# Kernel optimization log

Hardware: AMD Instinct MI355X
Metric: run time of the kernel (lower is better)

Reference implementation:

```python
import jax, jax.numpy as jnp
import numpy as np

B, H, L = 8, 256, 8192

def setup_inputs() -> dict:
    key = jax.random.key(0)
    k1, k2, k3 = jax.random.split(key, 3)
    u = jax.random.normal(k1, (B, H, L), dtype=jnp.float32)
    K = jax.random.normal(k2, (H, L), dtype=jnp.float32)
    # D ~ uniform_ring with min=max=1.0, field='real' -> random signs on unit ring
    D = jnp.where(jax.random.uniform(k3, (H,)) < 0.5, -1.0, 1.0).astype(jnp.float32)
    return {"u": u, "K": K, "D": D}

def reference(u, K, D):
    # FFT-based circular long convolution per channel: y = ifft(fft(u) * fft(K)).real
    u_s = jnp.fft.fft(u, axis=-1)            # (B,H,L) complex
    k_s = jnp.fft.fft(K, axis=-1)            # (H,L)   complex
    y = jnp.fft.ifft(u_s * k_s[None], axis=-1).real  # (B,H,L)
    y = y + D[None, :, None] * u             # skip connection D*u
    y = jnp.tanh(y)
    return y
```

## Files before the change

### kernel.cpp

```cpp
#include <hip/hip_runtime.h>
#include <math.h>


#define LL 8192
#define NT 512
#define HH 256
#define TWO_PI 6.2831853071795864f
#define CP8  0.92387953251129f
#define SP8  0.38268343236509f
#define CP4  0.70710678118654752f
#define SP4  0.70710678118654752f

__device__ __forceinline__ int SW(int e) {
    return e ^ ((e >> 4) & 0x18) ^ ((e >> 5) & 0x07);
}
__device__ __forceinline__ int SW2(int e) {
    return e ^ (((e >> 5) & 7) << 2);
}
__device__ __forceinline__ float fast_tanh(float x) {
    float e = __expf(2.0f * x);
    return 1.0f - 2.0f / (e + 1.0f);
}

template<int JT>
__device__ __forceinline__ void fill_pyr_cs(float c0, float s0, float Er, float Ei,
                                            float* twr, float* twi) {
    const int off = (1 << JT) - 1;
    twr[off] = c0; twi[off] = s0;
    #pragma unroll
    for (int m = 1; m < (1 << JT); ++m) {
        const float pr = twr[off + m - 1], pi = twi[off + m - 1];
        twr[off + m] = pr * Er - pi * Ei;
        twi[off + m] = pr * Ei + pi * Er;
    }
    #pragma unroll
    for (int j = JT - 1; j >= 0; --j) {
        #pragma unroll
        for (int m = 0; m < (1 << j); ++m) {
            const float a = twr[(2 << j) - 1 + m], b = twi[(2 << j) - 1 + m];
            twr[(1 << j) - 1 + m] = a * a - b * b;
            twi[(1 << j) - 1 + m] = 2.0f * a * b;
        }
    }
}
template<int JT>
__device__ __forceinline__ void fill_pyr(float ang0, float Er, float Ei,
                                         float* twr, float* twi) {
    float s, c;
    __sincosf(ang0, &s, &c);
    fill_pyr_cs<JT>(c, s, Er, Ei, twr, twi);
}

template<int R2>
__device__ __forceinline__ void dif_apply(float* xr, float* xi,
                                          const float* twr, const float* twi) {
    #pragma unroll
    for (int j = R2 - 1; j >= 0; --j) {
        #pragma unroll
        for (int q = 0; q < (1 << (R2 - 1)); ++q) {
            const int mm = q & ((1 << j) - 1);
            const int m0 = ((q >> j) << (j + 1)) | mm;
            const int m1 = m0 + (1 << j);
            const float wr = twr[(1 << j) - 1 + mm], wi = twi[(1 << j) - 1 + mm];
            const float ar = xr[m0], ai = xi[m0], br = xr[m1], bi = xi[m1];
            xr[m0] = ar + br; xi[m0] = ai + bi;
            const float dr = ar - br, di = ai - bi;
            xr[m1] = dr * wr - di * wi;
            xi[m1] = dr * wi + di * wr;
        }
    }
}
template<int R2>
__device__ __forceinline__ void dit_apply(float* xr, float* xi,
                                          const float* twr, const float* twi) {
    #pragma unroll
    for (int j = 0; j < R2; ++j) {
        #pragma unroll
        for (int q = 0; q < (1 << (R2 - 1)); ++q) {
            const int mm = q & ((1 << j) - 1);
            const int m0 = ((q >> j) << (j + 1)) | mm;
            const int m1 = m0 + (1 << j);
            const float wr = twr[(1 << j) - 1 + mm], wi = twi[(1 << j) - 1 + mm];
            const float br = xr[m1] * wr - xi[m1] * wi;
            const float bi = xr[m1] * wi + xi[m1] * wr;
            const float ar = xr[m0], ai = xi[m0];
            xr[m0] = ar + br; xi[m0] = ai + bi;
            xr[m1] = ar - br; xi[m1] = ai - bi;
        }
    }
}


__device__ __forceinline__ void fwd_A(float* xr, float* xi, int tid,
                                      float* re, float* im) {
    float twr[15], twi[15];
    fill_pyr<3>(-(TWO_PI / 8192.0f) * (float)tid, CP8, -SP8, twr, twi);
    dif_apply<4>(xr, xi, twr, twi);
    #pragma unroll
    for (int m = 0; m < 16; ++m) {
        const int p = SW(tid + (m << 9));
        re[p] = xr[m]; im[p] = xi[m];
    }
}

template<bool INV>
__device__ __forceinline__ void mid_M1(float* re, float* im, int lane, int wv) {
    float twr[7], twi[7];
    const float sgn = INV ? 1.0f : -1.0f;
    fill_pyr<2>(sgn * (TWO_PI / 512.0f) * (float)lane, CP4, sgn * SP4, twr, twi);
    #pragma unroll
    for (int r = 0; r < 2; ++r) {
        const int base = (((wv << 1) | r) << 9) + lane;
        float ar[8], ai[8];
        #pragma unroll
        for (int j = 0; j < 8; ++j) {
            const int p = SW(base + (j << 6));
            ar[j] = re[p]; ai[j] = im[p];
        }
        if (INV) dit_apply<3>(ar, ai, twr, twi);
        else     dif_apply<3>(ar, ai, twr, twi);
        #pragma unroll
        for (int j = 0; j < 8; ++j) {
            const int p = SW(base + (j << 6));
            re[p] = ar[j]; im[p] = ai[j];
        }
    }
}

template<bool INV>
__device__ __forceinline__ void mid_M2(float* re, float* im, int lane, int wv) {
    float twr[7], twi[7];
    const float sgn = INV ? 1.0f : -1.0f;
    fill_pyr<2>(sgn * (TWO_PI / 64.0f) * (float)(lane & 7), CP4, sgn * SP4, twr, twi);
    const int sub = ((lane >> 3) << 6) + (lane & 7);
    #pragma unroll
    for (int r = 0; r < 2; ++r) {
        const int base = (((wv << 1) | r) << 9) + sub;
        float ar[8], ai[8];
        #pragma unroll
        for (int j = 0; j < 8; ++j) {
            const int p = SW(base + (j << 3));
            ar[j] = re[p]; ai[j] = im[p];
        }
        if (INV) dit_apply<3>(ar, ai, twr, twi);
        else     dif_apply<3>(ar, ai, twr, twi);
        #pragma unroll
        for (int j = 0; j < 8; ++j) {
            const int p = SW(base + (j << 3));
            re[p] = ar[j]; im[p] = ai[j];
        }
    }
}

__global__ __launch_bounds__(NT, 4) void conv_kernel(const float* __restrict__ u,
                                                     const float2* __restrict__ Kf,
                                                     float* __restrict__ out) {
    __shared__ float re[LL];
    __shared__ float im[LL];
    const int tid = threadIdx.x;
    const int h = blockIdx.x & (HH - 1);
    const int pr_ = blockIdx.x >> 8;
    const size_t off0 = ((size_t)(pr_ * 2) * HH + h) * LL;
    const size_t off1 = off0 + (size_t)HH * LL;
    const float* u0 = u + off0;
    const float* u1 = u + off1;

    float xr[16], xi[16];
    #pragma unroll
    for (int m = 0; m < 16; ++m) {
        xr[m] = u0[tid + (m << 9)];
        xi[m] = u1[tid + (m << 9)];
    }
    fwd_A(xr, xi, tid, re, im);
    __syncthreads();

    const int lane = tid & 63, wv = tid >> 6;
    const int c0 = (wv << 1);

    float kwr[2][8], kwi[2][8];
    #pragma unroll
    for (int r = 0; r < 2; ++r) {
        const int eb = ((c0 | r) << 9) + (lane << 3);
        const float4* kp = (const float4*)(Kf + (size_t)h * LL + eb);
        #pragma unroll
        for (int jj = 0; jj < 4; ++jj) {
            const float4 v = kp[jj];
            kwr[r][2 * jj] = v.x;     kwi[r][2 * jj] = v.y;
            kwr[r][2 * jj + 1] = v.z; kwi[r][2 * jj + 1] = v.w;
        }
    }

    mid_M1<false>(re, im, lane, wv);
    mid_M2<false>(re, im, lane, wv);

    {
        float twd_r[7], twd_i[7], twu_r[7], twu_i[7];
        fill_pyr_cs<2>(1.0f, 0.0f, CP4, -SP4, twd_r, twd_i);
        fill_pyr_cs<2>(1.0f, 0.0f, CP4, SP4, twu_r, twu_i);
        #pragma unroll
        for (int r = 0; r < 2; ++r) {
            const int eb = ((c0 | r) << 9) + (lane << 3);
            float yr[8], yi[8];
            #pragma unroll
            for (int j = 0; j < 8; ++j) {
                const int p = SW(eb + j);
                yr[j] = re[p]; yi[j] = im[p];
            }
            dif_apply<3>(yr, yi, twd_r, twd_i);
            #pragma unroll
            for (int j = 0; j < 8; ++j) {
                const float a = yr[j], b = yi[j];
                yr[j] = a * kwr[r][j] - b * kwi[r][j];
                yi[j] = a * kwi[r][j] + b * kwr[r][j];
            }
            dit_apply<3>(yr, yi, twu_r, twu_i);
            #pragma unroll
            for (int j = 0; j < 8; ++j) {
                const int p = SW(eb + j);
                re[p] = yr[j]; im[p] = yi[j];
            }
        }
    }

    mid_M2<true>(re, im, lane, wv);
    mid_M1<true>(re, im, lane, wv);
    __syncthreads();

    {
        float twr[15], twi[15];
        #pragma unroll
        for (int m = 0; m < 16; ++m) {
            const int p = SW(tid + (m << 9));
            xr[m] = re[p]; xi[m] = im[p];
        }
        fill_pyr<3>((TWO_PI / 8192.0f) * (float)tid, CP8, SP8, twr, twi);
        dit_apply<4>(xr, xi, twr, twi);
    }
    float* o0 = out + off0;
    float* o1 = out + off1;
    #pragma unroll
    for (int m = 0; m < 16; ++m) {
        const int n = tid + (m << 9);
        o0[n] = fast_tanh(xr[m]);
        o1[n] = fast_tanh(xi[m]);
    }
}

__global__ __launch_bounds__(256) void kfftF_kernel(const float* __restrict__ K,
                                                    const float* __restrict__ D,
                                                    float2* __restrict__ Kf) {
    __shared__ float re[2048];
    __shared__ float im[2048];
    const int b = blockIdx.x;
    const int h = b >> 2, cq = b & 3;
    const int tid = threadIdx.x;
    const float* Kr = K + (size_t)h * LL;

    float xr[8], xi[8];
    #pragma unroll
    for (int j = 0; j < 8; ++j) {
        const int m = tid + (j << 8);
        const float A  = Kr[m];
        const float Bv = Kr[m + 2048];
        const float C  = Kr[m + 4096];
        const float E  = Kr[m + 6144];
        if (cq == 0) {
            xr[j] = A + C + Bv + E; xi[j] = 0.0f;
        } else {
            float sn, cs;
            __sincosf(-(TWO_PI / 8192.0f) * (float)m, &sn, &cs);
            if (cq == 1) {
                const float dif = A + C - Bv - E;
                const float c2 = cs * cs - sn * sn, s2 = 2.0f * cs * sn;
                xr[j] = dif * c2; xi[j] = dif * s2;
            } else {
                const float p_ = A - C, q_ = Bv - E;
                if (cq == 2) {
                    xr[j] = p_ * cs + q_ * sn; xi[j] = p_ * sn - q_ * cs;
                } else {
                    const float c2 = cs * cs - sn * sn, s2 = 2.0f * cs * sn;
                    const float c3 = cs * c2 - sn * s2, s3 = cs * s2 + sn * c2;
                    xr[j] = p_ * c3 - q_ * s3; xi[j] = p_ * s3 + q_ * c3;
                }
            }
        }
    }
    {
        float twr[7], twi[7];
        fill_pyr<2>(-(TWO_PI / 2048.0f) * (float)tid, CP4, -SP4, twr, twi);
        dif_apply<3>(xr, xi, twr, twi);
    }
    #pragma unroll
    for (int j = 0; j < 8; ++j) {
        const int p = SW2(tid + (j << 8));
        re[p] = xr[j]; im[p] = xi[j];
    }
    __syncthreads();
    {
        const int t_ = tid & 31, sub = tid >> 5;
        float twr[7], twi[7];
        fill_pyr<2>(-(TWO_PI / 256.0f) * (float)t_, CP4, -SP4, twr, twi);
        const int be = (sub << 8) + t_;
        float ar[8], ai[8];
        #pragma unroll
        for (int j = 0; j < 8; ++j) {
            const int p = SW2(be + (j << 5));
            ar[j] = re[p]; ai[j] = im[p];
        }
        dif_apply<3>(ar, ai, twr, twi);
        #pragma unroll
        for (int j = 0; j < 8; ++j) {
            const int p = SW2(be + (j << 5));
            re[p] = ar[j]; im[p] = ai[j];
        }
    }
    {
        const int blk = tid >> 2, r = tid & 3;
        float twr[7], twi[7];
        fill_pyr<2>(-(TWO_PI / 32.0f) * (float)r, CP4, -SP4, twr, twi);
        const int eb = (blk << 5) + r;
        float yr[8], yi[8];
        #pragma unroll
        for (int j = 0; j < 8; ++j) {
            const int p = SW2(eb + (j << 2));
            yr[j] = re[p]; yi[j] = im[p];
        }
        dif_apply<3>(yr, yi, twr, twi);
        const float s2_ = (r < 2) ? 1.0f : -1.0f;
        #pragma unroll
        for (int j = 0; j < 8; ++j) {
            const float vr = __shfl_xor(yr[j], 2);
            const float vi = __shfl_xor(yi[j], 2);
            const float tr = fmaf(yr[j], s2_, vr);
            const float ti = fmaf(yi[j], s2_, vi);
            yr[j] = (r == 3) ? ti : tr;
            yi[j] = (r == 3) ? -tr : ti;
        }
        const float s1_ = (r & 1) ? -1.0f : 1.0f;
        #pragma unroll
        for (int j = 0; j < 8; ++j) {
            const float vr = __shfl_xor(yr[j], 1);
            const float vi = __shfl_xor(yi[j], 1);
            yr[j] = fmaf(yr[j], s1_, vr);
            yi[j] = fmaf(yi[j], s1_, vi);
        }
        const float dh = D[h];
        const float invN = 1.0f / (float)LL;
        float2* baseo = Kf + (size_t)h * LL + (cq << 11);
        #pragma unroll
        for (int j = 0; j < 8; ++j) {
            baseo[eb + (j << 2)] = make_float2((yr[j] + dh) * invN, yi[j] * invN);
        }
    }
}

extern "C" void kernel_launch(void* const* d_in, const int* in_sizes, int n_in,
                              void* d_out, int out_size, void* d_ws, size_t ws_size,
                              hipStream_t stream) {
    const float* u = (const float*)d_in[0];
    const float* K = (const float*)d_in[1];
    const float* D = (const float*)d_in[2];
    float* out = (float*)d_out;
    float2* Kf = (float2*)d_ws;

    kfftF_kernel<<<dim3(4 * HH), dim3(256), 0, stream>>>(K, D, Kf);
    conv_kernel<<<dim3(4 * HH), dim3(NT), 0, stream>>>(u, Kf, out);
}
```

Measured before the change: 148.8 us.

## Process two batch pairs per block, reusing Kf spectrum and twiddles

Each conv_kernel block now handles two (batch-pair, channel) instances in a loop, halving the grid. The frequency-domain kernel coefficients are loaded once and reused across both instances. The forward mid-stage twiddles are also reused for the inverse pass via a conjugating DIT variant, which cuts twiddle recomputation. Launch bounds drop from 4 to 2 waves/SIMD-occupancy hint, trading parallelism (512 blocks) for fewer redundant loads and per-block setup.

```diff
diff --git a/kernel.cpp b/kernel.cpp
--- a/kernel.cpp
+++ b/kernel.cpp
@@ -89,6 +89,25 @@
         }
     }
 }
+template<int R2>
+__device__ __forceinline__ void dit_apply_c(float* xr, float* xi,
+                                            const float* twr, const float* twi) {
+    #pragma unroll
+    for (int j = 0; j < R2; ++j) {
+        #pragma unroll
+        for (int q = 0; q < (1 << (R2 - 1)); ++q) {
+            const int mm = q & ((1 << j) - 1);
+            const int m0 = ((q >> j) << (j + 1)) | mm;
+            const int m1 = m0 + (1 << j);
+            const float wr = twr[(1 << j) - 1 + mm], wi = -twi[(1 << j) - 1 + mm];
+            const float br = xr[m1] * wr - xi[m1] * wi;
+            const float bi = xr[m1] * wi + xi[m1] * wr;
+            const float ar = xr[m0], ai = xi[m0];
+            xr[m0] = ar + br; xi[m0] = ai + bi;
+            xr[m1] = ar - br; xi[m1] = ai - bi;
+        }
+    }
+}
 
 
 __device__ __forceinline__ void fwd_A(float* xr, float* xi, int tid,
@@ -104,10 +123,8 @@
 }
 
 template<bool INV>
-__device__ __forceinline__ void mid_M1(float* re, float* im, int lane, int wv) {
-    float twr[7], twi[7];
-    const float sgn = INV ? 1.0f : -1.0f;
-    fill_pyr<2>(sgn * (TWO_PI / 512.0f) * (float)lane, CP4, sgn * SP4, twr, twi);
+__device__ __forceinline__ void mid_M1p(float* re, float* im, int lane, int wv,
+                                        const float* twr, const float* twi) {
     #pragma unroll
     for (int r = 0; r < 2; ++r) {
         const int base = (((wv << 1) | r) << 9) + lane;
@@ -117,7 +134,7 @@
             const int p = SW(base + (j << 6));
             ar[j] = re[p]; ai[j] = im[p];
         }
-        if (INV) dit_apply<3>(ar, ai, twr, twi);
+        if (INV) dit_apply_c<3>(ar, ai, twr, twi);
         else     dif_apply<3>(ar, ai, twr, twi);
         #pragma unroll
         for (int j = 0; j < 8; ++j) {
@@ -128,10 +145,8 @@
 }
 
 template<bool INV>
-__device__ __forceinline__ void mid_M2(float* re, float* im, int lane, int wv) {
-    float twr[7], twi[7];
-    const float sgn = INV ? 1.0f : -1.0f;
-    fill_pyr<2>(sgn * (TWO_PI / 64.0f) * (float)(lane & 7), CP4, sgn * SP4, twr, twi);
+__device__ __forceinline__ void mid_M2p(float* re, float* im, int lane, int wv,
+                                        const float* twr, const float* twi) {
     const int sub = ((lane >> 3) << 6) + (lane & 7);
     #pragma unroll
     for (int r = 0; r < 2; ++r) {
@@ -142,7 +157,7 @@
             const int p = SW(base + (j << 3));
             ar[j] = re[p]; ai[j] = im[p];
         }
-        if (INV) dit_apply<3>(ar, ai, twr, twi);
+        if (INV) dit_apply_c<3>(ar, ai, twr, twi);
         else     dif_apply<3>(ar, ai, twr, twi);
         #pragma unroll
         for (int j = 0; j < 8; ++j) {
@@ -152,97 +167,110 @@
     }
 }
 
-__global__ __launch_bounds__(NT, 4) void conv_kernel(const float* __restrict__ u,
+__global__ __launch_bounds__(NT, 2) void conv_kernel(const float* __restrict__ u,
                                                      const float2* __restrict__ Kf,
                                                      float* __restrict__ out) {
     __shared__ float re[LL];
     __shared__ float im[LL];
     const int tid = threadIdx.x;
     const int h = blockIdx.x & (HH - 1);
-    const int pr_ = blockIdx.x >> 8;
-    const size_t off0 = ((size_t)(pr_ * 2) * HH + h) * LL;
-    const size_t off1 = off0 + (size_t)HH * LL;
-    const float* u0 = u + off0;
-    const float* u1 = u + off1;
-
-    float xr[16], xi[16];
-    #pragma unroll
-    for (int m = 0; m < 16; ++m) {
-        xr[m] = u0[tid + (m << 9)];
-        xi[m] = u1[tid + (m << 9)];
-    }
-    fwd_A(xr, xi, tid, re, im);
-    __syncthreads();
-
+    const int pr0 = blockIdx.x >> 8;
     const int lane = tid & 63, wv = tid >> 6;
     const int c0 = (wv << 1);
+    const float2* kf = Kf + (size_t)h * LL;
 
     float kwr[2][8], kwi[2][8];
-    #pragma unroll
-    for (int r = 0; r < 2; ++r) {
-        const int eb = ((c0 | r) << 9) + (lane << 3);
-        const float4* kp = (const float4*)(Kf + (size_t)h * LL + eb);
-        #pragma unroll
-        for (int jj = 0; jj < 4; ++jj) {
-            const float4 v = kp[jj];
-            kwr[r][2 * jj] = v.x;     kwi[r][2 * jj] = v.y;
-            kwr[r][2 * jj + 1] = v.z; kwi[r][2 * jj + 1] = v.w;
-        }
-    }
-
-    mid_M1<false>(re, im, lane, wv);
-    mid_M2<false>(re, im, lane, wv);
-
-    {
-        float twd_r[7], twd_i[7], twu_r[7], twu_i[7];
-        fill_pyr_cs<2>(1.0f, 0.0f, CP4, -SP4, twd_r, twd_i);
-        fill_pyr_cs<2>(1.0f, 0.0f, CP4, SP4, twu_r, twu_i);
-        #pragma unroll
-        for (int r = 0; r < 2; ++r) {
-            const int eb = ((c0 | r) << 9) + (lane << 3);
-            float yr[8], yi[8];
+
+    #pragma unroll
+    for (int inst = 0; inst < 2; ++inst) {
+        const int pr_ = pr0 + (inst << 1);
+        const size_t off0 = ((size_t)(pr_ * 2) * HH + h) * LL;
+        const size_t off1 = off0 + (size_t)HH * LL;
+        const float* u0 = u + off0;
+        const float* u1 = u + off1;
+
+        float xr[16], xi[16];
+        #pragma unroll
+        for (int m = 0; m < 16; ++m) {
+            xr[m] = u0[tid + (m << 9)];
+            xi[m] = u1[tid + (m << 9)];
+        }
+        if (inst) __syncthreads();
+        fwd_A(xr, xi, tid, re, im);
+        __syncthreads();
+
+        if (inst == 0) {
             #pragma unroll
-            for (int j = 0; j < 8; ++j) {
-                const int p = SW(eb + j);
-                yr[j] = re[p]; yi[j] = im[p];
+            for (int r = 0; r < 2; ++r) {
+                const int eb = ((c0 | r) << 9) + (lane << 3);
+                const float4* kp = (const float4*)(kf + eb);
+                #pragma unroll
+                for (int jj = 0; jj < 4; ++jj) {
+                    const float4 v = kp[jj];
+                    kwr[r][2 * jj] = v.x;     kwi[r][2 * jj] = v.y;
+                    kwr[r][2 * jj + 1] = v.z; kwi[r][2 * jj + 1] = v.w;
+                }
             }
-            dif_apply<3>(yr, yi, twd_r, twd_i);
+        }
+
+        float p1r[7], p1i[7];
+        fill_pyr<2>(-(TWO_PI / 512.0f) * (float)lane, CP4, -SP4, p1r, p1i);
+        mid_M1p<false>(re, im, lane, wv, p1r, p1i);
+
+        float p2r[7], p2i[7];
+        fill_pyr<2>(-(TWO_PI / 64.0f) * (float)(lane & 7), CP4, -SP4, p2r, p2i);
+        mid_M2p<false>(re, im, lane, wv, p2r, p2i);
+
+        {
+            float twd_r[7], twd_i[7];
+            fill_pyr_cs<2>(1.0f, 0.0f, CP4, -SP4, twd_r, twd_i);
             #pragma unroll
-            for (int j = 0; j < 8; ++j) {
-                const float a = yr[j], b = yi[j];
-                yr[j] = a * kwr[r][j] - b * kwi[r][j];
-                yi[j] = a * kwi[r][j] + b * kwr[r][j];
+            for (int r = 0; r < 2; ++r) {
+                const int eb = ((c0 | r) << 9) + (lane << 3);
+                float yr[8], yi[8];
+                #pragma unroll
+                for (int j = 0; j < 8; ++j) {
+                    const int p = SW(eb + j);
+                    yr[j] = re[p]; yi[j] = im[p];
+                }
+                dif_apply<3>(yr, yi, twd_r, twd_i);
+                #pragma unroll
+                for (int j = 0; j < 8; ++j) {
+                    const float a = yr[j], b = yi[j];
+                    yr[j] = a * kwr[r][j] - b * kwi[r][j];
+                    yi[j] = a * kwi[r][j] + b * kwr[r][j];
+                }
+                dit_apply_c<3>(yr, yi, twd_r, twd_i);
+                #pragma unroll
+                for (int j = 0; j < 8; ++j) {
+                    const int p = SW(eb + j);
+                    re[p] = yr[j]; im[p] = yi[j];
+                }
             }
-            dit_apply<3>(yr, yi, twu_r, twu_i);
+        }
+
+        mid_M2p<true>(re, im, lane, wv, p2r, p2i);
+        mid_M1p<true>(re, im, lane, wv, p1r, p1i);
+        __syncthreads();
+
+        {
+            float twr[15], twi[15];
             #pragma unroll
-            for (int j = 0; j < 8; ++j) {
-                const int p = SW(eb + j);
-                re[p] = yr[j]; im[p] = yi[j];
+            for (int m = 0; m < 16; ++m) {
+                const int p = SW(tid + (m << 9));
+                xr[m] = re[p]; xi[m] = im[p];
             }
-        }
-    }
-
-    mid_M2<true>(re, im, lane, wv);
-    mid_M1<true>(re, im, lane, wv);
-    __syncthreads();
-
-    {
-        float twr[15], twi[15];
+            fill_pyr<3>((TWO_PI / 8192.0f) * (float)tid, CP8, SP8, twr, twi);
+            dit_apply<4>(xr, xi, twr, twi);
+        }
+        float* o0 = out + off0;
+        float* o1 = out + off1;
         #pragma unroll
         for (int m = 0; m < 16; ++m) {
-            const int p = SW(tid + (m << 9));
-            xr[m] = re[p]; xi[m] = im[p];
-        }
-        fill_pyr<3>((TWO_PI / 8192.0f) * (float)tid, CP8, SP8, twr, twi);
-        dit_apply<4>(xr, xi, twr, twi);
-    }
-    float* o0 = out + off0;
-    float* o1 = out + off1;
-    #pragma unroll
-    for (int m = 0; m < 16; ++m) {
-        const int n = tid + (m << 9);
-        o0[n] = fast_tanh(xr[m]);
-        o1[n] = fast_tanh(xi[m]);
+            const int n = tid + (m << 9);
+            o0[n] = fast_tanh(xr[m]);
+            o1[n] = fast_tanh(xi[m]);
+        }
     }
 }
 
@@ -364,5 +392,5 @@
     float2* Kf = (float2*)d_ws;
 
     kfftF_kernel<<<dim3(4 * HH), dim3(256), 0, stream>>>(K, D, Kf);
-    conv_kernel<<<dim3(4 * HH), dim3(NT), 0, stream>>>(u, Kf, out);
-}
+    conv_kernel<<<dim3(2 * HH), dim3(NT), 0, stream>>>(u, Kf, out);
+}
```

Result: slower. 159.3 us (+7.1%).
